# Performance work log

Measured on AMD Instinct MI355X. Metric: run time of the kernel, lower is better.

The kernel has to match this reference:

```python
import jax, jax.numpy as jnp
import numpy as np

B, C, D, H, W = 8, 1, 128, 160, 128

def setup_inputs() -> dict:
    key = jax.random.key(0)
    kx, kb = jax.random.split(key)
    x = jax.random.normal(kx, (B, C, D, H, W), dtype=jnp.float32)
    base_volume = jax.random.normal(kb, (C, D, H, W), dtype=jnp.float32)
    return {"x": x, "base_volume": base_volume}

def reference(x, base_volume):
    # skimage match_histograms for continuous float images reduces (for a.e.-unique
    # values) to: map each source voxel's empirical CDF quantile onto the template's
    # inverse CDF via linear interpolation.
    tmpl = base_volume.ravel()
    t_sorted = jnp.sort(tmpl)                      # template inverse-CDF values
    M = tmpl.shape[0]
    tq = jnp.arange(1, M + 1, dtype=x.dtype) / M   # template CDF quantiles

    def match_one(sample):
        flat = sample.ravel()
        N = flat.shape[0]
        # rank of each voxel within its own sample (double argsort)
        ranks = jnp.argsort(jnp.argsort(flat))
        q = (ranks + 1).astype(flat.dtype) / N     # source empirical CDF
        matched = jnp.interp(q, tq, t_sorted)
        return matched.reshape(sample.shape)

    matched_vol = jax.vmap(match_one)(x)
    # self.model is identity here (the kernel headroom is the matching itself)
    return matched_vol
```

## Files before the change

kernel.cpp:

```cpp
#include <hip/hip_runtime.h>
#include <stdint.h>


#define SEG_N 2621440
#define NSEG 9
#define TILE 4096
#define NBLK (SEG_N / TILE)
#define RADIX 256
#define HL (RADIX * NBLK)
#define SCHUNK 4096
#define SNB (HL / SCHUNK)
#define SBUF (TILE + (TILE >> 4))

__device__ __forceinline__ uint32_t fkey(float f) {
  uint32_t b = __float_as_uint(f);
  return b ^ ((b & 0x80000000u) ? 0xFFFFFFFFu : 0x80000000u);
}
__device__ __forceinline__ float finv(uint32_t u) {
  uint32_t b = u ^ ((u & 0x80000000u) ? 0x80000000u : 0xFFFFFFFFu);
  return __uint_as_float(b);
}
__device__ __forceinline__ uint32_t SIDX(uint32_t i) { return i + (i >> 4); }

__global__ __launch_bounds__(256) void init_k(const float* __restrict__ x,
                                              const float* __restrict__ tmpl,
                                              int segbase,
                                              uint64_t* __restrict__ pairsA,
                                              uint32_t* __restrict__ Hkb) {
  __shared__ uint32_t hw[4 * RADIX];
  const int t = threadIdx.x;
  const int blk = blockIdx.x;
  const int sl = blockIdx.y;
  const int seg = segbase + sl;
  const float* src = (seg == 0) ? tmpl : (x + (size_t)(seg - 1) * SEG_N);
  uint64_t* pa = pairsA + (size_t)sl * SEG_N;
  hw[t] = 0; hw[t + 256] = 0; hw[t + 512] = 0; hw[t + 768] = 0;
  __syncthreads();
  const int w = t >> 6;
  const uint32_t base = blk * TILE;
  const float4* s4 = reinterpret_cast<const float4*>(src + base);
#pragma unroll
  for (int r = 0; r < 4; ++r) {
    float4 v = s4[r * 256 + t];
    uint32_t i0 = base + (uint32_t)(r * 256 + t) * 4u;
    float f[4] = {v.x, v.y, v.z, v.w};
#pragma unroll
    for (int c = 0; c < 4; ++c) {
      uint32_t k = fkey(f[c]);
      atomicAdd(&hw[w * 256 + (k & 255u)], 1u);
      pa[i0 + c] = ((uint64_t)k << 32) | (uint64_t)(i0 + c);
    }
  }
  __syncthreads();
  Hkb[(size_t)sl * HL + (size_t)blk * RADIX + t] =
      hw[t] + hw[t + 256] + hw[t + 512] + hw[t + 768];
}

__device__ __forceinline__ void wf_count(uint32_t d, uint32_t* hist) {
  const int lane = threadIdx.x & 63;
  uint64_t rem = ~0ull;
  while (rem) {
    uint32_t lead = (uint32_t)__ffsll((unsigned long long)rem) - 1u;
    uint32_t d0 = (uint32_t)__shfl((int)d, (int)lead, 64);
    uint64_t eq = __ballot(d == d0);
    if (lane == (int)lead) atomicAdd(&hist[d0], (uint32_t)__popcll(eq));
    rem &= ~eq;
  }
}

template <int P>
__global__ __launch_bounds__(256) void hist_k(const uint64_t* __restrict__ pairs,
                                              uint32_t* __restrict__ Hkb) {
  __shared__ uint32_t hw[4 * RADIX];
  const int t = threadIdx.x;
  const int blk = blockIdx.x;
  const int sl = blockIdx.y;
  hw[t] = 0; hw[t + 256] = 0; hw[t + 512] = 0; hw[t + 768] = 0;
  __syncthreads();
  const int w = t >> 6;
  const int sh = 32 + 8 * P;
  const ulonglong2* pc = reinterpret_cast<const ulonglong2*>(
      pairs + (size_t)sl * SEG_N + (size_t)blk * TILE);
#pragma unroll
  for (int r = 0; r < 8; ++r) {
    ulonglong2 v = pc[r * 256 + t];
    uint32_t d0 = (uint32_t)(v.x >> sh) & 255u;
    uint32_t d1 = (uint32_t)(v.y >> sh) & 255u;
    if (P == 3) {
      wf_count(d0, &hw[w * 256]);
      wf_count(d1, &hw[w * 256]);
    } else {
      atomicAdd(&hw[w * 256 + d0], 1u);
      atomicAdd(&hw[w * 256 + d1], 1u);
    }
  }
  __syncthreads();
  Hkb[(size_t)sl * HL + (size_t)blk * RADIX + t] =
      hw[t] + hw[t + 256] + hw[t + 512] + hw[t + 768];
}

__global__ __launch_bounds__(256) void scanT_k(const uint32_t* __restrict__ Hkb,
                                               uint32_t* __restrict__ Hbk,
                                               uint32_t* __restrict__ desc) {
  __shared__ uint32_t lds[256];
  __shared__ uint32_t baseS;
  const int t = threadIdx.x;
  const int c = blockIdx.x;
  const int sl = blockIdx.y;
  const uint32_t* src = Hkb + (size_t)sl * HL;
  const uint32_t e0 = (uint32_t)c * SCHUNK + (uint32_t)t * 16;
  uint32_t vals[16];
  uint32_t s = 0;
#pragma unroll
  for (int i = 0; i < 16; ++i) {
    uint32_t e = e0 + (uint32_t)i;
    uint32_t bin = e / NBLK, blk = e - bin * NBLK;
    vals[i] = src[(size_t)blk * RADIX + bin];
    s += vals[i];
  }
  lds[t] = s;
  __syncthreads();
#pragma unroll
  for (int off = 1; off < 256; off <<= 1) {
    uint32_t a = (t >= off) ? lds[t - off] : 0u;
    __syncthreads();
    lds[t] += a;
    __syncthreads();
  }
  const uint32_t incl = lds[t];
  const uint32_t total = lds[255];
  const uint32_t ex = incl - s;

  uint32_t* dseg = desc + sl * SNB;
  if (t == 0) {
    __hip_atomic_store(&dseg[c], (total & 0x3FFFFFFFu) |
                                     ((c == 0 ? 2u : 1u) << 30),
                       __ATOMIC_RELAXED, __HIP_MEMORY_SCOPE_AGENT);
    uint32_t acc = 0;
    if (c > 0) {
      int b = c - 1;
      bool done = false;
      while (!done) {
        uint32_t dv[8];
        const int n = (b >= 7) ? 8 : (b + 1);
#pragma unroll
        for (int i = 0; i < 8; ++i)
          if (i < n)
            dv[i] = __hip_atomic_load(&dseg[b - i], __ATOMIC_RELAXED,
                                      __HIP_MEMORY_SCOPE_AGENT);
        for (int i = 0; i < n; ++i) {
          uint32_t v = dv[i];
          while ((v >> 30) == 0u)
            v = __hip_atomic_load(&dseg[b - i], __ATOMIC_RELAXED,
                                  __HIP_MEMORY_SCOPE_AGENT);
          acc += v & 0x3FFFFFFFu;
          if ((v >> 30) == 2u) { done = true; break; }
        }
        b -= n;
        if (!done && b < 0) break;
      }
      __hip_atomic_store(&dseg[c], ((acc + total) & 0x3FFFFFFFu) | (2u << 30),
                         __ATOMIC_RELAXED, __HIP_MEMORY_SCOPE_AGENT);
    }
    baseS = acc;
  }
  __syncthreads();
  uint32_t run = baseS + ex;
  uint32_t* dst = Hbk + (size_t)sl * HL + e0;
#pragma unroll
  for (int i = 0; i < 16; ++i) {
    dst[i] = run;
    run += vals[i];
  }
}

__device__ __forceinline__ void scan_pack2(uint32_t v0, uint32_t v1, uint32_t* s,
                                           uint32_t& ex0, uint32_t& ex1,
                                           uint32_t& tot0, uint32_t& tot1) {
  const int lane = threadIdx.x & 63, w = threadIdx.x >> 6;
  uint32_t a = v0, b = v1;
#pragma unroll
  for (int o = 1; o < 64; o <<= 1) {
    uint32_t na = __shfl_up(a, (unsigned)o, 64);
    uint32_t nb = __shfl_up(b, (unsigned)o, 64);
    if (lane >= o) { a += na; b += nb; }
  }
  if (lane == 63) { s[w] = a; s[4 + w] = b; }
  __syncthreads();
  if (threadIdx.x == 0) {
    uint32_t r0 = 0, r1 = 0;
#pragma unroll
    for (int i = 0; i < 4; ++i) {
      uint32_t q0 = s[i], q1 = s[4 + i];
      s[i] = r0; s[4 + i] = r1;
      r0 += q0; r1 += q1;
    }
    s[8] = r0; s[9] = r1;
  }
  __syncthreads();
  ex0 = a - v0 + s[w];
  ex1 = b - v1 + s[4 + w];
  tot0 = s[8]; tot1 = s[9];
  __syncthreads();
}

template <int P, int MODE>
__global__ __launch_bounds__(256) void part_k(const uint64_t* __restrict__ src,
                                              uint64_t* __restrict__ dst,
                                              const uint32_t* __restrict__ Hbk,
                                              float* __restrict__ tsorted,
                                              float* __restrict__ out,
                                              int segbase, int slbase) {
  __shared__ uint64_t buf[SBUF];
  __shared__ uint32_t ldsStart[RADIX];
  __shared__ uint32_t ldsBase[RADIX];
  __shared__ uint32_t scanS[12];
  const int t = threadIdx.x;
  const int blk = blockIdx.x;
  const int sl = slbase + blockIdx.y;
  const int seg = segbase + sl;
  const uint64_t* ps = src + (size_t)sl * SEG_N + (size_t)blk * TILE;

  ldsBase[t] = Hbk[(size_t)sl * HL + (size_t)t * NBLK + blk];

#pragma unroll
  for (int r = 0; r < 16; ++r) buf[SIDX(r * 256 + t)] = ps[r * 256 + t];
  __syncthreads();

  uint64_t e[16];
#pragma unroll
  for (int rnd = 0; rnd < 4; ++rnd) {
#pragma unroll
    for (int j = 0; j < 16; ++j) e[j] = buf[SIDX(t * 16 + j)];
    uint32_t cnt[4] = {0u, 0u, 0u, 0u};
#pragma unroll
    for (int j = 0; j < 16; ++j) {
      uint32_t d2 = (uint32_t)(e[j] >> (32 + 8 * P + 2 * rnd)) & 3u;
      cnt[d2]++;
    }
    uint32_t p0 = cnt[0] | (cnt[1] << 16);
    uint32_t p1 = cnt[2] | (cnt[3] << 16);
    uint32_t ex0, ex1, tot0, tot1;
    scan_pack2(p0, p1, scanS, ex0, ex1, tot0, tot1);
    uint32_t t0 = tot0 & 0xffffu, t1 = tot0 >> 16, t2 = tot1 & 0xffffu;
    uint32_t pos[4];
    pos[0] = (ex0 & 0xffffu);
    pos[1] = t0 + (ex0 >> 16);
    pos[2] = t0 + t1 + (ex1 & 0xffffu);
    pos[3] = t0 + t1 + t2 + (ex1 >> 16);
#pragma unroll
    for (int j = 0; j < 16; ++j) {
      uint32_t d2 = (uint32_t)(e[j] >> (32 + 8 * P + 2 * rnd)) & 3u;
      buf[SIDX(pos[d2]++)] = e[j];
    }
    __syncthreads();
  }

  const uint8_t* b8 = reinterpret_cast<const uint8_t*>(buf);
#pragma unroll
  for (int r = 0; r < 16; ++r) {
    uint32_t s = (uint32_t)(r * 256 + t);
    e[r] = buf[SIDX(s)];
    uint32_t d = (uint32_t)(e[r] >> (32 + 8 * P)) & 255u;
    uint32_t dp = (s == 0) ? 0x100u
                           : (uint32_t)b8[(size_t)SIDX(s - 1) * 8 + 4 + P];
    if (d != dp) ldsStart[d] = s;
  }
  __syncthreads();

#pragma unroll
  for (int r = 0; r < 16; ++r) {
    uint32_t s = (uint32_t)(r * 256 + t);
    uint64_t el = e[r];
    uint32_t key = (uint32_t)(el >> 32);
    uint32_t d = (key >> (8 * P)) & 255u;
    uint32_t dest = ldsBase[d] + s - ldsStart[d];
    if (MODE == 0) {
      dst[(size_t)sl * SEG_N + dest] = el;
    } else if (MODE == 1) {
      tsorted[dest] = finv(key);
    } else {
      out[(size_t)(seg - 1) * SEG_N + (uint32_t)el] = tsorted[dest];
    }
  }
}

extern "C" void kernel_launch(void* const* d_in, const int* in_sizes, int n_in,
                              void* d_out, int out_size, void* d_ws, size_t ws_size,
                              hipStream_t stream) {
  const float* x = (const float*)d_in[0];
  const float* tmpl = (const float*)d_in[1];
  float* out = (float*)d_out;

  auto need = [](int nb) -> size_t {
    return (size_t)nb * ((size_t)SEG_N * 16 + (size_t)HL * 8 + 4096) +
           (size_t)SEG_N * 4 + 16384;
  };
  const int nb = (ws_size >= need(9)) ? 9 : (ws_size >= need(3)) ? 3 : 1;

  uint8_t* w = (uint8_t*)d_ws;
  size_t off = 0;
  auto carve = [&](size_t bytes) -> void* {
    void* p = w + off;
    off = (off + bytes + 255) & ~(size_t)255;
    return p;
  };
  uint64_t* pairsA = (uint64_t*)carve((size_t)nb * SEG_N * 8);
  uint64_t* pairsB = (uint64_t*)carve((size_t)nb * SEG_N * 8);
  uint32_t* Hkb = (uint32_t*)carve((size_t)nb * HL * 4);
  uint32_t* Hbk = (uint32_t*)carve((size_t)nb * HL * 4);
  uint32_t* desc = (uint32_t*)carve((size_t)4 * nb * SNB * 4);
  float* tsorted = (float*)carve((size_t)SEG_N * 4);

  for (int g = 0; g < NSEG; g += nb) {
    const dim3 gi(NBLK, nb);
    const dim3 gs(SNB, nb);

    hipMemsetAsync(desc, 0, (size_t)4 * nb * SNB * 4, stream);

    init_k<<<gi, 256, 0, stream>>>(x, tmpl, g, pairsA, Hkb);
    scanT_k<<<gs, 256, 0, stream>>>(Hkb, Hbk, desc + 0 * nb * SNB);
    part_k<0, 0><<<gi, 256, 0, stream>>>(pairsA, pairsB, Hbk, tsorted, out, g, 0);
    hist_k<1><<<gi, 256, 0, stream>>>(pairsB, Hkb);
    scanT_k<<<gs, 256, 0, stream>>>(Hkb, Hbk, desc + 1 * nb * SNB);
    part_k<1, 0><<<gi, 256, 0, stream>>>(pairsB, pairsA, Hbk, tsorted, out, g, 0);
    hist_k<2><<<gi, 256, 0, stream>>>(pairsA, Hkb);
    scanT_k<<<gs, 256, 0, stream>>>(Hkb, Hbk, desc + 2 * nb * SNB);
    part_k<2, 0><<<gi, 256, 0, stream>>>(pairsA, pairsB, Hbk, tsorted, out, g, 0);
    hist_k<3><<<gi, 256, 0, stream>>>(pairsB, Hkb);
    scanT_k<<<gs, 256, 0, stream>>>(Hkb, Hbk, desc + 3 * nb * SNB);
    if (g == 0) {
      part_k<3, 1><<<dim3(NBLK, 1), 256, 0, stream>>>(pairsB, pairsA, Hbk,
                                                      tsorted, out, g, 0);
      if (nb > 1)
        part_k<3, 2><<<dim3(NBLK, nb - 1), 256, 0, stream>>>(pairsB, pairsA, Hbk,
                                                             tsorted, out, g, 1);
    } else {
      part_k<3, 2><<<dim3(NBLK, nb), 256, 0, stream>>>(pairsB, pairsA, Hbk,
                                                       tsorted, out, g, 0);
    }
  }
}
```

Before: 1.185 ms.

## Fuse key-pair construction into first partition pass and store histograms bin-major

The first histogram kernel now reads the floats and only counts digits, and the first partition pass builds the key/index pairs from the raw floats in shared memory. This avoids writing and re-reading a full pairs buffer. Histograms are written directly in bin-major layout, so the scan reads and writes contiguous vectors in place and the extra histogram buffer is dropped. The wavefront-aggregated counting for the top digit is replaced by plain shared atomics, which may contend more on skewed exponent bytes.

```diff
diff --git a/kernel.cpp b/kernel.cpp
--- a/kernel.cpp
+++ b/kernel.cpp
@@ -22,55 +22,35 @@
 }
 __device__ __forceinline__ uint32_t SIDX(uint32_t i) { return i + (i >> 4); }
 
-__global__ __launch_bounds__(256) void init_k(const float* __restrict__ x,
-                                              const float* __restrict__ tmpl,
-                                              int segbase,
-                                              uint64_t* __restrict__ pairsA,
-                                              uint32_t* __restrict__ Hkb) {
+__global__ __launch_bounds__(256) void hist0_k(const float* __restrict__ x,
+                                               const float* __restrict__ tmpl,
+                                               int segbase,
+                                               uint32_t* __restrict__ Hbk) {
   __shared__ uint32_t hw[4 * RADIX];
   const int t = threadIdx.x;
   const int blk = blockIdx.x;
   const int sl = blockIdx.y;
   const int seg = segbase + sl;
   const float* src = (seg == 0) ? tmpl : (x + (size_t)(seg - 1) * SEG_N);
-  uint64_t* pa = pairsA + (size_t)sl * SEG_N;
   hw[t] = 0; hw[t + 256] = 0; hw[t + 512] = 0; hw[t + 768] = 0;
   __syncthreads();
   const int w = t >> 6;
-  const uint32_t base = blk * TILE;
-  const float4* s4 = reinterpret_cast<const float4*>(src + base);
+  const float4* s4 = reinterpret_cast<const float4*>(src + blk * TILE);
 #pragma unroll
   for (int r = 0; r < 4; ++r) {
     float4 v = s4[r * 256 + t];
-    uint32_t i0 = base + (uint32_t)(r * 256 + t) * 4u;
     float f[4] = {v.x, v.y, v.z, v.w};
 #pragma unroll
-    for (int c = 0; c < 4; ++c) {
-      uint32_t k = fkey(f[c]);
-      atomicAdd(&hw[w * 256 + (k & 255u)], 1u);
-      pa[i0 + c] = ((uint64_t)k << 32) | (uint64_t)(i0 + c);
-    }
-  }
-  __syncthreads();
-  Hkb[(size_t)sl * HL + (size_t)blk * RADIX + t] =
+    for (int c = 0; c < 4; ++c)
+      atomicAdd(&hw[w * 256 + (fkey(f[c]) & 255u)], 1u);
+  }
+  __syncthreads();
+  Hbk[(size_t)sl * HL + (size_t)t * NBLK + blk] =
       hw[t] + hw[t + 256] + hw[t + 512] + hw[t + 768];
 }
 
-__device__ __forceinline__ void wf_count(uint32_t d, uint32_t* hist) {
-  const int lane = threadIdx.x & 63;
-  uint64_t rem = ~0ull;
-  while (rem) {
-    uint32_t lead = (uint32_t)__ffsll((unsigned long long)rem) - 1u;
-    uint32_t d0 = (uint32_t)__shfl((int)d, (int)lead, 64);
-    uint64_t eq = __ballot(d == d0);
-    if (lane == (int)lead) atomicAdd(&hist[d0], (uint32_t)__popcll(eq));
-    rem &= ~eq;
-  }
-}
-
-template <int P>
 __global__ __launch_bounds__(256) void hist_k(const uint64_t* __restrict__ pairs,
-                                              uint32_t* __restrict__ Hkb) {
+                                              uint32_t* __restrict__ Hbk, int p) {
   __shared__ uint32_t hw[4 * RADIX];
   const int t = threadIdx.x;
   const int blk = blockIdx.x;
@@ -78,53 +58,43 @@
   hw[t] = 0; hw[t + 256] = 0; hw[t + 512] = 0; hw[t + 768] = 0;
   __syncthreads();
   const int w = t >> 6;
-  const int sh = 32 + 8 * P;
+  const int sh = 32 + 8 * p;
   const ulonglong2* pc = reinterpret_cast<const ulonglong2*>(
       pairs + (size_t)sl * SEG_N + (size_t)blk * TILE);
 #pragma unroll
   for (int r = 0; r < 8; ++r) {
     ulonglong2 v = pc[r * 256 + t];
-    uint32_t d0 = (uint32_t)(v.x >> sh) & 255u;
-    uint32_t d1 = (uint32_t)(v.y >> sh) & 255u;
-    if (P == 3) {
-      wf_count(d0, &hw[w * 256]);
-      wf_count(d1, &hw[w * 256]);
-    } else {
-      atomicAdd(&hw[w * 256 + d0], 1u);
-      atomicAdd(&hw[w * 256 + d1], 1u);
-    }
-  }
-  __syncthreads();
-  Hkb[(size_t)sl * HL + (size_t)blk * RADIX + t] =
+    atomicAdd(&hw[w * 256 + ((uint32_t)(v.x >> sh) & 255u)], 1u);
+    atomicAdd(&hw[w * 256 + ((uint32_t)(v.y >> sh) & 255u)], 1u);
+  }
+  __syncthreads();
+  Hbk[(size_t)sl * HL + (size_t)t * NBLK + blk] =
       hw[t] + hw[t + 256] + hw[t + 512] + hw[t + 768];
 }
 
-__global__ __launch_bounds__(256) void scanT_k(const uint32_t* __restrict__ Hkb,
-                                               uint32_t* __restrict__ Hbk,
+__global__ __launch_bounds__(256) void scanT_k(uint32_t* __restrict__ Hbk,
                                                uint32_t* __restrict__ desc) {
   __shared__ uint32_t lds[256];
   __shared__ uint32_t baseS;
   const int t = threadIdx.x;
   const int c = blockIdx.x;
   const int sl = blockIdx.y;
-  const uint32_t* src = Hkb + (size_t)sl * HL;
-  const uint32_t e0 = (uint32_t)c * SCHUNK + (uint32_t)t * 16;
-  uint32_t vals[16];
+  uint32_t* base = Hbk + (size_t)sl * HL + (size_t)c * SCHUNK + (size_t)t * 16;
+  uint4* p4 = reinterpret_cast<uint4*>(base);
+  uint4 a[4];
   uint32_t s = 0;
 #pragma unroll
-  for (int i = 0; i < 16; ++i) {
-    uint32_t e = e0 + (uint32_t)i;
-    uint32_t bin = e / NBLK, blk = e - bin * NBLK;
-    vals[i] = src[(size_t)blk * RADIX + bin];
-    s += vals[i];
+  for (int k = 0; k < 4; ++k) {
+    a[k] = p4[k];
+    s += a[k].x + a[k].y + a[k].z + a[k].w;
   }
   lds[t] = s;
   __syncthreads();
 #pragma unroll
   for (int off = 1; off < 256; off <<= 1) {
-    uint32_t a = (t >= off) ? lds[t - off] : 0u;
+    uint32_t v = (t >= off) ? lds[t - off] : 0u;
     __syncthreads();
-    lds[t] += a;
+    lds[t] += v;
     __syncthreads();
   }
   const uint32_t incl = lds[t];
@@ -166,11 +136,14 @@
   }
   __syncthreads();
   uint32_t run = baseS + ex;
-  uint32_t* dst = Hbk + (size_t)sl * HL + e0;
-#pragma unroll
-  for (int i = 0; i < 16; ++i) {
-    dst[i] = run;
-    run += vals[i];
+#pragma unroll
+  for (int k = 0; k < 4; ++k) {
+    uint4 o;
+    o.x = run; run += a[k].x;
+    o.y = run; run += a[k].y;
+    o.z = run; run += a[k].z;
+    o.w = run; run += a[k].w;
+    p4[k] = o;
   }
 }
 
@@ -208,6 +181,8 @@
 __global__ __launch_bounds__(256) void part_k(const uint64_t* __restrict__ src,
                                               uint64_t* __restrict__ dst,
                                               const uint32_t* __restrict__ Hbk,
+                                              const float* __restrict__ xin,
+                                              const float* __restrict__ tmplin,
                                               float* __restrict__ tsorted,
                                               float* __restrict__ out,
                                               int segbase, int slbase) {
@@ -219,12 +194,31 @@
   const int blk = blockIdx.x;
   const int sl = slbase + blockIdx.y;
   const int seg = segbase + sl;
-  const uint64_t* ps = src + (size_t)sl * SEG_N + (size_t)blk * TILE;
 
   ldsBase[t] = Hbk[(size_t)sl * HL + (size_t)t * NBLK + blk];
 
-#pragma unroll
-  for (int r = 0; r < 16; ++r) buf[SIDX(r * 256 + t)] = ps[r * 256 + t];
+  if (MODE == 3) {
+    const float* fsrc =
+        (seg == 0) ? tmplin : (xin + (size_t)(seg - 1) * SEG_N);
+    const float4* s4 = reinterpret_cast<const float4*>(fsrc + blk * TILE);
+    const uint32_t base = (uint32_t)blk * TILE;
+#pragma unroll
+    for (int r = 0; r < 4; ++r) {
+      float4 v = s4[r * 256 + t];
+      uint32_t i0 = base + (uint32_t)(r * 256 + t) * 4u;
+      float f[4] = {v.x, v.y, v.z, v.w};
+#pragma unroll
+      for (int c = 0; c < 4; ++c) {
+        uint32_t k = fkey(f[c]);
+        buf[SIDX((uint32_t)(r * 256 + t) * 4u + (uint32_t)c)] =
+            ((uint64_t)k << 32) | (uint64_t)(i0 + c);
+      }
+    }
+  } else {
+    const uint64_t* ps = src + (size_t)sl * SEG_N + (size_t)blk * TILE;
+#pragma unroll
+    for (int r = 0; r < 16; ++r) buf[SIDX(r * 256 + t)] = ps[r * 256 + t];
+  }
   __syncthreads();
 
   uint64_t e[16];
@@ -275,7 +269,7 @@
     uint32_t key = (uint32_t)(el >> 32);
     uint32_t d = (key >> (8 * P)) & 255u;
     uint32_t dest = ldsBase[d] + s - ldsStart[d];
-    if (MODE == 0) {
+    if (MODE == 0 || MODE == 3) {
       dst[(size_t)sl * SEG_N + dest] = el;
     } else if (MODE == 1) {
       tsorted[dest] = finv(key);
@@ -293,7 +287,7 @@
   float* out = (float*)d_out;
 
   auto need = [](int nb) -> size_t {
-    return (size_t)nb * ((size_t)SEG_N * 16 + (size_t)HL * 8 + 4096) +
+    return (size_t)nb * ((size_t)SEG_N * 16 + (size_t)HL * 4 + 4096) +
            (size_t)SEG_N * 4 + 16384;
   };
   const int nb = (ws_size >= need(9)) ? 9 : (ws_size >= need(3)) ? 3 : 1;
@@ -307,7 +301,6 @@
   };
   uint64_t* pairsA = (uint64_t*)carve((size_t)nb * SEG_N * 8);
   uint64_t* pairsB = (uint64_t*)carve((size_t)nb * SEG_N * 8);
-  uint32_t* Hkb = (uint32_t*)carve((size_t)nb * HL * 4);
   uint32_t* Hbk = (uint32_t*)carve((size_t)nb * HL * 4);
   uint32_t* desc = (uint32_t*)carve((size_t)4 * nb * SNB * 4);
   float* tsorted = (float*)carve((size_t)SEG_N * 4);
@@ -318,26 +311,29 @@
 
     hipMemsetAsync(desc, 0, (size_t)4 * nb * SNB * 4, stream);
 
-    init_k<<<gi, 256, 0, stream>>>(x, tmpl, g, pairsA, Hkb);
-    scanT_k<<<gs, 256, 0, stream>>>(Hkb, Hbk, desc + 0 * nb * SNB);
-    part_k<0, 0><<<gi, 256, 0, stream>>>(pairsA, pairsB, Hbk, tsorted, out, g, 0);
-    hist_k<1><<<gi, 256, 0, stream>>>(pairsB, Hkb);
-    scanT_k<<<gs, 256, 0, stream>>>(Hkb, Hbk, desc + 1 * nb * SNB);
-    part_k<1, 0><<<gi, 256, 0, stream>>>(pairsB, pairsA, Hbk, tsorted, out, g, 0);
-    hist_k<2><<<gi, 256, 0, stream>>>(pairsA, Hkb);
-    scanT_k<<<gs, 256, 0, stream>>>(Hkb, Hbk, desc + 2 * nb * SNB);
-    part_k<2, 0><<<gi, 256, 0, stream>>>(pairsA, pairsB, Hbk, tsorted, out, g, 0);
-    hist_k<3><<<gi, 256, 0, stream>>>(pairsB, Hkb);
-    scanT_k<<<gs, 256, 0, stream>>>(Hkb, Hbk, desc + 3 * nb * SNB);
+    hist0_k<<<gi, 256, 0, stream>>>(x, tmpl, g, Hbk);
+    scanT_k<<<gs, 256, 0, stream>>>(Hbk, desc + 0 * nb * SNB);
+    part_k<0, 3><<<gi, 256, 0, stream>>>(nullptr, pairsA, Hbk, x, tmpl,
+                                         tsorted, out, g, 0);
+    hist_k<<<gi, 256, 0, stream>>>(pairsA, Hbk, 1);
+    scanT_k<<<gs, 256, 0, stream>>>(Hbk, desc + 1 * nb * SNB);
+    part_k<1, 0><<<gi, 256, 0, stream>>>(pairsA, pairsB, Hbk, nullptr, nullptr,
+                                         tsorted, out, g, 0);
+    hist_k<<<gi, 256, 0, stream>>>(pairsB, Hbk, 2);
+    scanT_k<<<gs, 256, 0, stream>>>(Hbk, desc + 2 * nb * SNB);
+    part_k<2, 0><<<gi, 256, 0, stream>>>(pairsB, pairsA, Hbk, nullptr, nullptr,
+                                         tsorted, out, g, 0);
+    hist_k<<<gi, 256, 0, stream>>>(pairsA, Hbk, 3);
+    scanT_k<<<gs, 256, 0, stream>>>(Hbk, desc + 3 * nb * SNB);
     if (g == 0) {
-      part_k<3, 1><<<dim3(NBLK, 1), 256, 0, stream>>>(pairsB, pairsA, Hbk,
-                                                      tsorted, out, g, 0);
+      part_k<3, 1><<<dim3(NBLK, 1), 256, 0, stream>>>(
+          pairsA, pairsB, Hbk, nullptr, nullptr, tsorted, out, g, 0);
       if (nb > 1)
-        part_k<3, 2><<<dim3(NBLK, nb - 1), 256, 0, stream>>>(pairsB, pairsA, Hbk,
-                                                             tsorted, out, g, 1);
+        part_k<3, 2><<<dim3(NBLK, nb - 1), 256, 0, stream>>>(
+            pairsA, pairsB, Hbk, nullptr, nullptr, tsorted, out, g, 1);
     } else {
-      part_k<3, 2><<<dim3(NBLK, nb), 256, 0, stream>>>(pairsB, pairsA, Hbk,
-                                                       tsorted, out, g, 0);
-    }
-  }
-}
+      part_k<3, 2><<<dim3(NBLK, nb), 256, 0, stream>>>(
+          pairsA, pairsB, Hbk, nullptr, nullptr, tsorted, out, g, 0);
+    }
+  }
+}
```

Result: faster. 1.104 ms (-6.8%).
